# Performance work log

Measured on AMD Instinct MI355X. Metric: run time of the kernel, lower is better.

Reference implementation:

```python
import jax, jax.numpy as jnp
import numpy as np

EPS = 1e-5

def conv(x, w, groups=1):
    # x: NCHW, w: OIHW, VALID padding, stride 1 (cross-correlation, same as torch conv2d)
    return jax.lax.conv_general_dilated(x, w, (1, 1), 'VALID',
                                        feature_group_count=groups,
                                        dimension_numbers=('NCHW', 'OIHW', 'NCHW'))

def bn(x, g, b, m, v):
    # eval-mode batchnorm with running stats
    scale = (g / jnp.sqrt(v + EPS))[None, :, None, None]
    return (x - m[None, :, None, None]) * scale + b[None, :, None, None]

def xcorr_depthwise(x, k):
    # x: [B,C,Hs,Ws] search, k: [B,C,Hk,Wk] per-sample kernels
    B, C, H, W = x.shape
    xr = x.reshape(1, B * C, H, W)
    kr = k.reshape(B * C, 1, k.shape[2], k.shape[3])
    out = conv(xr, kr, groups=B * C)  # [1, B*C, Ho, Wo]
    return out.reshape(B, C, out.shape[2], out.shape[3])

def setup_inputs() -> dict:
    key = jax.random.key(0)
    ks = jax.random.split(key, 16)
    Cin, Hid, Cout = 256, 256, 20
    inp = {
        'kernel': jax.random.normal(ks[0], (128, Cin, 7, 7), jnp.float32),
        'search': jax.random.normal(ks[1], (128, Cin, 31, 31), jnp.float32),
        'wk': jax.random.normal(ks[2], (Hid, Cin, 3, 3), jnp.float32) * 0.02,
        'gk': jnp.ones((Hid,), jnp.float32),
        'bk': jnp.zeros((Hid,), jnp.float32),
        'mk': jax.random.normal(ks[3], (Hid,), jnp.float32) * 0.1,
        'vk': jax.random.uniform(ks[4], (Hid,), jnp.float32) + 0.5,
        'ws': jax.random.normal(ks[5], (Hid, Cin, 3, 3), jnp.float32) * 0.02,
        'gs': jnp.ones((Hid,), jnp.float32),
        'bs': jnp.zeros((Hid,), jnp.float32),
        'ms': jax.random.normal(ks[6], (Hid,), jnp.float32) * 0.1,
        'vs': jax.random.uniform(ks[7], (Hid,), jnp.float32) + 0.5,
        'wh1': jax.random.normal(ks[8], (Hid, Hid, 1, 1), jnp.float32) * 0.02,
        'gh': jnp.ones((Hid,), jnp.float32),
        'bh': jnp.zeros((Hid,), jnp.float32),
        'mh': jax.random.normal(ks[9], (Hid,), jnp.float32) * 0.1,
        'vh': jax.random.uniform(ks[10], (Hid,), jnp.float32) + 0.5,
        'wh2': jax.random.normal(ks[11], (Cout, Hid, 1, 1), jnp.float32) * 0.02,
        'bh2': jnp.zeros((Cout,), jnp.float32),
    }
    return inp

def reference(kernel, search, wk, gk, bk, mk, vk, ws, gs, bs, ms, vs,
              wh1, gh, bh, mh, vh, wh2, bh2):
    k = jax.nn.relu(bn(conv(kernel, wk), gk, bk, mk, vk))   # [B,256,5,5]
    s = jax.nn.relu(bn(conv(search, ws), gs, bs, ms, vs))   # [B,256,29,29]
    f = xcorr_depthwise(s, k)                               # [B,256,25,25]
    h = jax.nn.relu(bn(conv(f, wh1), gh, bh, mh, vh))
    out = conv(h, wh2) + bh2[None, :, None, None]           # [B,20,25,25]
    return out
```

## Files before the change

### kernel.cpp

```cpp
#include <hip/hip_runtime.h>

typedef __bf16 bf16x8 __attribute__((ext_vector_type(8)));
typedef float floatx4 __attribute__((ext_vector_type(4)));
typedef unsigned short u16;
typedef unsigned int u32;

__device__ __forceinline__ u16 f2bf(float f) {
    union { float f; unsigned int u; } q; q.f = f;
    unsigned int r = q.u + 0x7FFFu + ((q.u >> 16) & 1u);
    return (u16)(r >> 16);
}
__device__ __forceinline__ float bf2f(u16 b) {
    union { unsigned int u; float f; } q; q.u = ((unsigned int)b) << 16;
    return q.f;
}

__device__ __forceinline__ void gl2lds16(const u16* g, u16* l) {
    __builtin_amdgcn_global_load_lds((const __attribute__((address_space(1))) u32*)g,
                                     (__attribute__((address_space(3))) u32*)l, 16, 0, 0);
}

__global__ __launch_bounds__(256) void prep_and_transpose(
    const float* __restrict__ kin, u16* __restrict__ KIN,
    const float* __restrict__ sin_, u16* __restrict__ SIN,
    const float* __restrict__ wk, const float* __restrict__ wsw, const float* __restrict__ wh1,
    const float* __restrict__ gk, const float* __restrict__ bk,
    const float* __restrict__ mk, const float* __restrict__ vk,
    const float* __restrict__ gs, const float* __restrict__ bs,
    const float* __restrict__ ms, const float* __restrict__ vs,
    const float* __restrict__ gh, const float* __restrict__ bh,
    const float* __restrict__ mh, const float* __restrict__ vh,
    u16* __restrict__ WKP, u16* __restrict__ WSP, u16* __restrict__ WH1P,
    float* __restrict__ par)
{
    __shared__ float tile[64][33];
    int bid = blockIdx.x, t = threadIdx.x;
    if (bid < 16896) {
        const float* in; u16* out; int HW, sptiles;
        if (bid < 1024) { in = kin;  out = KIN; HW = 49;  sptiles = 2; }
        else { bid -= 1024; in = sin_; out = SIN; HW = 961; sptiles = 31; }
        int st  = bid % sptiles;
        int tmp = bid / sptiles;
        int ct  = tmp & 3;
        int b   = tmp >> 2;
        int sp0 = st * 32, ci0 = ct * 64;
        int j = t & 31, i8 = t >> 5;
        const float* ip = in + ((size_t)b * 256 + ci0 + i8) * HW + sp0 + j;
#pragma unroll
        for (int k = 0; k < 8; ++k) {
            if (sp0 + j < HW) tile[i8 + k * 8][j] = ip[(size_t)(k * 8) * HW];
        }
        __syncthreads();
        int cl = t & 63, s4 = t >> 6;
#pragma unroll
        for (int k = 0; k < 8; ++k) {
            int spl = s4 + k * 4;
            int sp  = sp0 + spl;
            if (sp < HW) out[((size_t)b * HW + sp) * 256 + ci0 + cl] = f2bf(tile[cl][spl]);
        }
        return;
    }
    bid -= 16896;
    if (bid < 4608) {
        const float* src = (bid < 2304) ? wk : wsw;
        u16* dst = (bid < 2304) ? WKP : WSP;
        int tid = ((bid < 2304) ? bid : bid - 2304) * 256 + t;
        int o  = tid / 2304;
        int k  = tid - o * 2304;
        int rc = k >> 8;
        int ci = k & 255;
        dst[tid] = f2bf(src[o * 2304 + ci * 9 + rc]);
    } else if (bid < 4864) {
        int tid = (bid - 4608) * 256 + t;
        WH1P[tid] = f2bf(wh1[tid]);
    } else {
        float s;
        s = gk[t] * rsqrtf(vk[t] + 1e-5f); par[0*256+t] = s; par[1*256+t] = bk[t] - mk[t]*s;
        s = gs[t] * rsqrtf(vs[t] + 1e-5f); par[2*256+t] = s; par[3*256+t] = bs[t] - ms[t]*s;
        s = gh[t] * rsqrtf(vh[t] + 1e-5f); par[4*256+t] = s; par[5*256+t] = bh[t] - mh[t]*s;
    }
}

__global__ __launch_bounds__(256) void conv_gemm(
    const u16* __restrict__ Ain, const u16* __restrict__ Wpk,
    const float* __restrict__ scale, const float* __restrict__ shift,
    u16* __restrict__ Out,
    int OHW, int OW, int IW, int bstride, int KW, int nrc, int mblocks)
{
    __shared__ u16 Alds[4096];
    __shared__ u16 Blds[4096];

    const int tot = mblocks * 2;
    const int grp = (tot >> 3) << 3;
    const int lid = blockIdx.x;
    const int nid = (lid < grp) ? ((lid & 7) * (grp >> 3) + (lid >> 3)) : lid;
    const int m0 = (nid >> 1) * 128;
    const int n0 = (nid & 1) * 128;

    const int t    = threadIdx.x;
    const int wave = t >> 6;
    const int lane = t & 63;
    const int quad = lane >> 4;
    const int lrow = lane & 15;

    const int koff = (((t & 3) ^ ((t >> 3) & 3)) << 3);
    const int r0 = t >> 2;
    int m_a0 = m0 + r0;
    int b0 = m_a0 / OHW; int rem0 = m_a0 - b0 * OHW; int y0 = rem0 / OW; int x0 = rem0 - y0 * OW;
    int m_a1 = m_a0 + 64;
    int b1 = m_a1 / OHW; int rem1 = m_a1 - b1 * OHW; int y1 = rem1 / OW; int x1 = rem1 - y1 * OW;
    const u16* ag0 = Ain + (size_t)b0 * bstride + (size_t)(y0 * IW + x0) * 256 + koff;
    const u16* ag1 = Ain + (size_t)b1 * bstride + (size_t)(y1 * IW + x1) * 256 + koff;
    const int Ktot = nrc * 256;
    const u16* bg0 = Wpk + (size_t)(n0 + r0) * Ktot + koff;
    const u16* bg1 = bg0 + (size_t)64 * Ktot;

    u16* lA0 = Alds + wave * 512;
    u16* lA1 = Alds + 2048 + wave * 512;
    u16* lB0 = Blds + wave * 512;
    u16* lB1 = Blds + 2048 + wave * 512;

    floatx4 zero = {0.f, 0.f, 0.f, 0.f};
    floatx4 acc[4][4];
#pragma unroll
    for (int i = 0; i < 4; ++i)
#pragma unroll
        for (int j = 0; j < 4; ++j) acc[i][j] = zero;

    const int wr  = (wave >> 1) << 6;
    const int wc  = (wave & 1) << 6;
    const int pos = ((quad ^ ((lrow >> 1) & 3)) << 3);

    const int nchunks = nrc << 3;
    for (int ch = 0; ch < nchunks; ++ch) {
        int rc  = ch >> 3;
        int ci0 = (ch & 7) << 5;
        int rr  = rc / KW;
        int cc  = rc - rr * KW;
        int ao  = (rr * IW + cc) * 256 + ci0;
        int bo  = ch << 5;
        __syncthreads();
        gl2lds16(ag0 + ao, lA0);
        gl2lds16(ag1 + ao, lA1);
        gl2lds16(bg0 + bo, lB0);
        gl2lds16(bg1 + bo, lB1);
        __syncthreads();
        bf16x8 af[4], bfr[4];
#pragma unroll
        for (int mi = 0; mi < 4; ++mi)
            af[mi] = *(const bf16x8*)&Alds[(wr + mi * 16 + lrow) * 32 + pos];
#pragma unroll
        for (int ni = 0; ni < 4; ++ni)
            bfr[ni] = *(const bf16x8*)&Blds[(wc + ni * 16 + lrow) * 32 + pos];
#pragma unroll
        for (int mi = 0; mi < 4; ++mi)
#pragma unroll
            for (int ni = 0; ni < 4; ++ni)
                acc[mi][ni] = __builtin_amdgcn_mfma_f32_16x16x32_bf16(af[mi], bfr[ni], acc[mi][ni], 0, 0, 0);
    }

    float sc[4], sh[4];
#pragma unroll
    for (int ni = 0; ni < 4; ++ni) {
        int gn = n0 + wc + ni * 16 + lrow;
        sc[ni] = scale[gn];
        sh[ni] = shift[gn];
    }
#pragma unroll
    for (int mi = 0; mi < 4; ++mi) {
        int gm = m0 + wr + mi * 16 + (quad << 2);
#pragma unroll
        for (int ri = 0; ri < 4; ++ri) {
            size_t ro = (size_t)(gm + ri) * 256 + n0 + wc + lrow;
#pragma unroll
            for (int ni = 0; ni < 4; ++ni) {
                float v = acc[mi][ni][ri] * sc[ni] + sh[ni];
                v = fmaxf(v, 0.f);
                Out[ro + ni * 16] = f2bf(v);
            }
        }
    }
}

#define NS_BLK 421
__global__ __launch_bounds__(512, 2) void conv_gemm256(
    const u16* __restrict__ AinS, const u16* __restrict__ WpkS,
    const float* __restrict__ parS, u16* __restrict__ OutS,
    const u16* __restrict__ AinK, const u16* __restrict__ WpkK,
    const float* __restrict__ parK, u16* __restrict__ OutK)
{
    __shared__ __align__(16) u16 Alds[2][256][64];
    __shared__ __align__(16) u16 Blds[2][256][64];

    const int Ktot = 2304;
    const int NKT  = 36;
    const int KW   = 3;

    const int lid = blockIdx.x;
    const bool isk = (lid >= NS_BLK);

    int nid;
    if (!isk) {
        const int xcd = lid & 7, sub = lid >> 3;
        nid = (xcd < 5) ? (xcd * 53 + sub) : (265 + (xcd - 5) * 52 + sub);
    } else {
        nid = lid - NS_BLK;
    }
    const int m0 = nid << 8;

    const int OHW     = isk ? 25    : 841;
    const int OW      = isk ? 5     : 29;
    const int IW      = isk ? 7     : 31;
    const int bstride = isk ? 12544 : 246016;
    const int Mtot    = isk ? 3200  : 107648;
    const u16* Ain    = isk ? AinK : AinS;
    const u16* Wpk    = isk ? WpkK : WpkS;
    const float* scale = isk ? parK : parS;
    const float* shift = scale + 256;
    u16* Out          = isk ? OutK : OutS;

    const int t     = threadIdx.x;
    const int wave  = t >> 6;
    const int lane  = t & 63;
    const int lrow  = lane & 15;
    const int lquad = lane >> 4;
    const int wmBase = (wave >> 2) << 7;
    const int wnBase = (wave & 3) << 6;

    const u16* pA[4];
    const u16* pB[4];
#pragma unroll
    for (int j = 0; j < 4; ++j) {
        int u = j * 512 + t;
        int row = u >> 3, slot = u & 7;
        int ko = ((slot ^ (row & 7)) << 3);
        int m = m0 + row; if (m >= Mtot) m = Mtot - 1;
        int b = m / OHW; int rem = m - b * OHW; int y = rem / OW; int x = rem - y * OW;
        pA[j] = Ain + (size_t)b * bstride + (size_t)(y * IW + x) * 256 + ko;
        pB[j] = Wpk + (size_t)row * (size_t)Ktot + ko;
    }

    const int xo0 = ((lquad ^ (lrow & 7)) << 3);
    const int xo1 = xo0 ^ 32;

    floatx4 acc[8][4];
#pragma unroll
    for (int i = 0; i < 8; ++i)
#pragma unroll
        for (int j = 0; j < 4; ++j) acc[i][j] = (floatx4){0.f, 0.f, 0.f, 0.f};

#pragma unroll
    for (int j = 0; j < 4; ++j)
        gl2lds16(pA[j], &Alds[0][0][0] + j * 4096 + wave * 512);
#pragma unroll
    for (int j = 0; j < 4; ++j)
        gl2lds16(pB[j], &Blds[0][0][0] + j * 4096 + wave * 512);
    asm volatile("s_waitcnt vmcnt(0)" ::: "memory");
    __builtin_amdgcn_s_barrier();

#define LOADA(mb) do {                                              \
        const u16* _p = Ab + (wmBase + (mb) * 16 + lrow) * 64;      \
        aF[0][0] = *(const bf16x8*)(_p + xo0);                      \
        aF[0][1] = *(const bf16x8*)(_p + xo1);                      \
        aF[1][0] = *(const bf16x8*)(_p + 1024 + xo0);               \
        aF[1][1] = *(const bf16x8*)(_p + 1024 + xo1);               \
    } while (0)

#define MFMA16(mb) do {                                                                               \
        _Pragma("unroll")                                                                             \
        for (int _n = 0; _n < 4; ++_n) {                                                              \
            acc[(mb)][_n]     = __builtin_amdgcn_mfma_f32_16x16x32_bf16(aF[0][0], bB[_n][0], acc[(mb)][_n], 0, 0, 0);     \
            acc[(mb)][_n]     = __builtin_amdgcn_mfma_f32_16x16x32_bf16(aF[0][1], bB[_n][1], acc[(mb)][_n], 0, 0, 0);     \
            acc[(mb) + 1][_n] = __builtin_amdgcn_mfma_f32_16x16x32_bf16(aF[1][0], bB[_n][0], acc[(mb) + 1][_n], 0, 0, 0); \
            acc[(mb) + 1][_n] = __builtin_amdgcn_mfma_f32_16x16x32_bf16(aF[1][1], bB[_n][1], acc[(mb) + 1][_n], 0, 0, 0); \
        }                                                                                             \
    } while (0)

#pragma unroll 2
    for (int kt = 0; kt < NKT; ++kt) {
        const int c = kt & 1;
        const u16* Ab = &Alds[c][0][0];
        const u16* Bb = &Blds[c][0][0];
        u16* An = &Alds[c ^ 1][0][0];
        u16* Bn = &Blds[c ^ 1][0][0];
        const int pf = (kt + 1 < NKT);
        const int kt1 = kt + 1;
        const int rc = kt1 >> 2;
        const int rr = rc / KW;
        const int cc = rc - rr * KW;
        const int aoffA = (rr * IW + cc) * 256 + ((kt1 & 3) << 6);
        const int boffB = kt1 << 6;

        if (pf) {
#pragma unroll
            for (int j = 0; j < 4; ++j)
                gl2lds16(pA[j] + aoffA, An + j * 4096 + wave * 512);
#pragma unroll
            for (int j = 0; j < 4; ++j)
                gl2lds16(pB[j] + boffB, Bn + j * 4096 + wave * 512);
        }

        bf16x8 bB[4][2];
        bf16x8 aF[2][2];
#pragma unroll
        for (int ni = 0; ni < 4; ++ni) {
            const u16* _p = Bb + (wnBase + ni * 16 + lrow) * 64;
            bB[ni][0] = *(const bf16x8*)(_p + xo0);
            bB[ni][1] = *(const bf16x8*)(_p + xo1);
        }
        LOADA(0);
        MFMA16(0);
        LOADA(2);
        MFMA16(2);
        LOADA(4);
        MFMA16(4);
        LOADA(6);
        MFMA16(6);

        asm volatile("s_waitcnt vmcnt(0)" ::: "memory");
        __builtin_amdgcn_s_barrier();
    }

#undef LOADA
#undef MFMA16

    float sc[4], sh[4];
#pragma unroll
    for (int ni = 0; ni < 4; ++ni) {
        int gn = wnBase + ni * 16 + lrow;
        sc[ni] = scale[gn];
        sh[ni] = shift[gn];
    }
#pragma unroll
    for (int mi = 0; mi < 8; ++mi) {
        int gm0 = m0 + wmBase + mi * 16 + (lquad << 2);
#pragma unroll
        for (int ri = 0; ri < 4; ++ri) {
            int gm = gm0 + ri;
            if (gm < Mtot) {
                size_t ro = (size_t)gm * 256 + wnBase + lrow;
#pragma unroll
                for (int ni = 0; ni < 4; ++ni) {
                    float v = acc[mi][ni][ri] * sc[ni] + sh[ni];
                    v = fmaxf(v, 0.f);
                    Out[ro + ni * 16] = f2bf(v);
                }
            }
        }
    }
}

__global__ __launch_bounds__(256) void xcorr(const u16* __restrict__ ss, const u16* __restrict__ kk,
                                             u16* __restrict__ f) {
    int lid = blockIdx.x;
    int bid = (lid & 7) * 400 + (lid >> 3);
    int b = bid / 25, y = bid - b * 25;
    int t = threadIdx.x;
    int cg = (t & 31) << 3;
    int xg = t >> 5;
    const u16* kbase = kk + (size_t)b * 25 * 256 + cg;
    const u16* sbase = ss + (size_t)(b * 29 + y) * 29 * 256 + cg;

    float acc[4][8];
#pragma unroll
    for (int j = 0; j < 4; ++j)
#pragma unroll
        for (int e = 0; e < 8; ++e) acc[j][e] = 0.f;

#pragma unroll
    for (int r = 0; r < 5; ++r) {
        const u16* srow = sbase + (size_t)r * 29 * 256;
#pragma unroll
        for (int c = 0; c < 5; ++c) {
            bf16x8 kv = *(const bf16x8*)(kbase + (r * 5 + c) * 256);
            float kf[8];
#pragma unroll
            for (int e = 0; e < 8; ++e) kf[e] = (float)kv[e];
#pragma unroll
            for (int j = 0; j < 4; ++j) {
                int x = xg + 8 * j;
                if (x < 25) {
                    bf16x8 sv = *(const bf16x8*)(srow + (size_t)(x + c) * 256);
#pragma unroll
                    for (int e = 0; e < 8; ++e) acc[j][e] += (float)sv[e] * kf[e];
                }
            }
        }
    }

    u16* fb = f + (size_t)(b * 25 + y) * 25 * 256 + cg;
#pragma unroll
    for (int j = 0; j < 4; ++j) {
        int x = xg + 8 * j;
        if (x < 25) {
            u16 pk[8];
#pragma unroll
            for (int e = 0; e < 8; ++e) pk[e] = f2bf(acc[j][e]);
            *(bf16x8*)(fb + (size_t)x * 256) = *(const bf16x8*)pk;
        }
    }
}

__global__ __launch_bounds__(256) void head(const u16* __restrict__ h, const float* __restrict__ w2,
                                            const float* __restrict__ b2, float* __restrict__ out) {
    __shared__ __align__(16) u16   hl[25 * 264];
    __shared__ __align__(16) float wl[20 * 260];
    int bid = blockIdx.x;
    int b = bid / 25, y = bid - b * 25;
    int t = threadIdx.x;
    const u16* hrow = h + (size_t)(b * 25 + y) * 25 * 256;
    for (int i = t; i < 800; i += 256) {
        int x = i >> 5, c8 = i & 31;
        *(bf16x8*)&hl[x * 264 + c8 * 8] = *(const bf16x8*)&hrow[i * 8];
    }
    for (int i = t; i < 1280; i += 256) {
        int co = i >> 6, c4 = i & 63;
        *(float4*)&wl[co * 260 + c4 * 4] = *(const float4*)&w2[(size_t)co * 256 + c4 * 4];
    }
    __syncthreads();
    for (int o = t; o < 500; o += 256) {
        int x = o / 20, co = o - x * 20;
        float acc = b2[co];
        const u16* hp = &hl[x * 264];
        const float* wp = &wl[co * 260];
#pragma unroll 4
        for (int k = 0; k < 256; k += 8) {
            bf16x8 hv = *(const bf16x8*)(hp + k);
            float4 w0 = *(const float4*)(wp + k);
            float4 w1v = *(const float4*)(wp + k + 4);
            acc += (float)hv[0] * w0.x + (float)hv[1] * w0.y
                 + (float)hv[2] * w0.z + (float)hv[3] * w0.w
                 + (float)hv[4] * w1v.x + (float)hv[5] * w1v.y
                 + (float)hv[6] * w1v.z + (float)hv[7] * w1v.w;
        }
        out[(size_t)((b * 20 + co) * 25 + y) * 25 + x] = acc;
    }
}

#define OFF_SIN  0ull
#define SZ_SIN   62980096ull
#define OFF_KIN  (OFF_SIN + SZ_SIN)
#define SZ_KIN   3211264ull
#define OFF_WKP  (OFF_KIN + SZ_KIN)
#define SZ_WKP   1179648ull
#define OFF_WSP  (OFF_WKP + SZ_WKP)
#define SZ_WSP   1179648ull
#define OFF_WH1P (OFF_WSP + SZ_WSP)
#define SZ_WH1P  131072ull
#define OFF_PAR  (OFF_WH1P + SZ_WH1P)
#define SZ_PAR   8192ull
#define OFF_KK   (OFF_PAR + SZ_PAR)
#define SZ_KK    1638400ull
#define OFF_SS   (OFF_KK + SZ_KK)
#define SZ_SS    55115776ull
#define OFF_F    OFF_SIN
#define OFF_H    OFF_SS

extern "C" void kernel_launch(void* const* d_in, const int* in_sizes, int n_in,
                              void* d_out, int out_size, void* d_ws, size_t ws_size,
                              hipStream_t stream) {
    const float* kin  = (const float*)d_in[0];
    const float* sin_ = (const float*)d_in[1];
    const float* wk   = (const float*)d_in[2];
    const float* gk   = (const float*)d_in[3];
    const float* bk   = (const float*)d_in[4];
    const float* mk   = (const float*)d_in[5];
    const float* vk   = (const float*)d_in[6];
    const float* wsw  = (const float*)d_in[7];
    const float* gs   = (const float*)d_in[8];
    const float* bs   = (const float*)d_in[9];
    const float* ms   = (const float*)d_in[10];
    const float* vs   = (const float*)d_in[11];
    const float* wh1  = (const float*)d_in[12];
    const float* gh   = (const float*)d_in[13];
    const float* bh   = (const float*)d_in[14];
    const float* mh   = (const float*)d_in[15];
    const float* vh   = (const float*)d_in[16];
    const float* wh2  = (const float*)d_in[17];
    const float* bh2  = (const float*)d_in[18];
    float* out = (float*)d_out;

    char* w = (char*)d_ws;
    u16*   SIN  = (u16*)(w + OFF_SIN);
    u16*   KIN  = (u16*)(w + OFF_KIN);
    u16*   WKP  = (u16*)(w + OFF_WKP);
    u16*   WSP  = (u16*)(w + OFF_WSP);
    u16*   WH1P = (u16*)(w + OFF_WH1P);
    float* PAR  = (float*)(w + OFF_PAR);
    u16*   KK   = (u16*)(w + OFF_KK);
    u16*   SS   = (u16*)(w + OFF_SS);
    u16*   F    = (u16*)(w + OFF_F);
    u16*   H    = (u16*)(w + OFF_H);

    prep_and_transpose<<<21761, 256, 0, stream>>>(kin, KIN, sin_, SIN,
                                                  wk, wsw, wh1,
                                                  gk, bk, mk, vk, gs, bs, ms, vs, gh, bh, mh, vh,
                                                  WKP, WSP, WH1P, PAR);

    conv_gemm256<<<434, 512, 0, stream>>>(SIN, WSP, PAR + 512, SS,
                                          KIN, WKP, PAR + 0, KK);
    xcorr<<<3200, 256, 0, stream>>>(SS, KK, F);
    conv_gemm<<<1250, 256, 0, stream>>>(F, WH1P, PAR + 1024, PAR + 1280, H,
                                        625, 25, 25, 160000, 1, 1, 625);
    head<<<3200, 256, 0, stream>>>(H, wh2, bh2, out);

    (void)in_sizes; (void)n_in; (void)out_size; (void)ws_size;
}
```

Measured before the change: 484.9 us.

## Shrink conv GEMM tile to 256x128 with K32 steps for higher occupancy

```diff
diff --git a/kernel.cpp b/kernel.cpp
--- a/kernel.cpp
+++ b/kernel.cpp
@@ -182,19 +182,18 @@
     }
 }
 
-#define NS_BLK 421
-__global__ __launch_bounds__(512, 2) void conv_gemm256(
+#define NS_BLK 842
+__global__ __launch_bounds__(512, 4) void conv_gemm256(
     const u16* __restrict__ AinS, const u16* __restrict__ WpkS,
     const float* __restrict__ parS, u16* __restrict__ OutS,
     const u16* __restrict__ AinK, const u16* __restrict__ WpkK,
     const float* __restrict__ parK, u16* __restrict__ OutK)
 {
-    __shared__ __align__(16) u16 Alds[2][256][64];
-    __shared__ __align__(16) u16 Blds[2][256][64];
+    __shared__ __align__(16) u16 Alds[2][256][32];
+    __shared__ __align__(16) u16 Blds[2][128][32];
 
     const int Ktot = 2304;
-    const int NKT  = 36;
-    const int KW   = 3;
+    const int NKT  = 72;
 
     const int lid = blockIdx.x;
     const bool isk = (lid >= NS_BLK);
@@ -202,11 +201,12 @@
     int nid;
     if (!isk) {
         const int xcd = lid & 7, sub = lid >> 3;
-        nid = (xcd < 5) ? (xcd * 53 + sub) : (265 + (xcd - 5) * 52 + sub);
+        nid = (xcd < 2) ? (xcd * 106 + sub) : (212 + (xcd - 2) * 105 + sub);
     } else {
         nid = lid - NS_BLK;
     }
-    const int m0 = nid << 8;
+    const int m0 = (nid >> 1) << 8;
+    const int n0 = (nid & 1) << 7;
 
     const int OHW     = isk ? 25    : 841;
     const int OW      = isk ? 5     : 29;
@@ -224,57 +224,39 @@
     const int lane  = t & 63;
     const int lrow  = lane & 15;
     const int lquad = lane >> 4;
-    const int wmBase = (wave >> 2) << 7;
-    const int wnBase = (wave & 3) << 6;
-
-    const u16* pA[4];
-    const u16* pB[4];
-#pragma unroll
-    for (int j = 0; j < 4; ++j) {
+    const int wmBase = (wave >> 1) << 6;
+    const int wnBase = (wave & 1) << 6;
+
+    const u16* pA[2];
+#pragma unroll
+    for (int j = 0; j < 2; ++j) {
         int u = j * 512 + t;
-        int row = u >> 3, slot = u & 7;
-        int ko = ((slot ^ (row & 7)) << 3);
+        int row = u >> 2, slot = u & 3;
+        int ko = ((slot ^ (row & 3) ^ ((row >> 2) & 3)) << 3);
         int m = m0 + row; if (m >= Mtot) m = Mtot - 1;
         int b = m / OHW; int rem = m - b * OHW; int y = rem / OW; int x = rem - y * OW;
         pA[j] = Ain + (size_t)b * bstride + (size_t)(y * IW + x) * 256 + ko;
-        pB[j] = Wpk + (size_t)row * (size_t)Ktot + ko;
-    }
-
-    const int xo0 = ((lquad ^ (lrow & 7)) << 3);
-    const int xo1 = xo0 ^ 32;
-
-    floatx4 acc[8][4];
-#pragma unroll
-    for (int i = 0; i < 8; ++i)
+    }
+    const u16* pB;
+    {
+        int row = t >> 2, slot = t & 3;
+        int ko = ((slot ^ (row & 3) ^ ((row >> 2) & 3)) << 3);
+        pB = Wpk + (size_t)(n0 + row) * Ktot + ko;
+    }
+
+    const int xo = ((lquad ^ (lrow & 3) ^ ((lrow >> 2) & 3)) << 3);
+
+    floatx4 acc[4][4];
+#pragma unroll
+    for (int i = 0; i < 4; ++i)
 #pragma unroll
         for (int j = 0; j < 4; ++j) acc[i][j] = (floatx4){0.f, 0.f, 0.f, 0.f};
 
-#pragma unroll
-    for (int j = 0; j < 4; ++j)
-        gl2lds16(pA[j], &Alds[0][0][0] + j * 4096 + wave * 512);
-#pragma unroll
-    for (int j = 0; j < 4; ++j)
-        gl2lds16(pB[j], &Blds[0][0][0] + j * 4096 + wave * 512);
+    gl2lds16(pA[0], &Alds[0][0][0] + 0 * 4096 + wave * 512);
+    gl2lds16(pA[1], &Alds[0][0][0] + 1 * 4096 + wave * 512);
+    gl2lds16(pB,    &Blds[0][0][0] + wave * 512);
     asm volatile("s_waitcnt vmcnt(0)" ::: "memory");
     __builtin_amdgcn_s_barrier();
-
-#define LOADA(mb) do {                                              \
-        const u16* _p = Ab + (wmBase + (mb) * 16 + lrow) * 64;      \
-        aF[0][0] = *(const bf16x8*)(_p + xo0);                      \
-        aF[0][1] = *(const bf16x8*)(_p + xo1);                      \
-        aF[1][0] = *(const bf16x8*)(_p + 1024 + xo0);               \
-        aF[1][1] = *(const bf16x8*)(_p + 1024 + xo1);               \
-    } while (0)
-
-#define MFMA16(mb) do {                                                                               \
-        _Pragma("unroll")                                                                             \
-        for (int _n = 0; _n < 4; ++_n) {                                                              \
-            acc[(mb)][_n]     = __builtin_amdgcn_mfma_f32_16x16x32_bf16(aF[0][0], bB[_n][0], acc[(mb)][_n], 0, 0, 0);     \
-            acc[(mb)][_n]     = __builtin_amdgcn_mfma_f32_16x16x32_bf16(aF[0][1], bB[_n][1], acc[(mb)][_n], 0, 0, 0);     \
-            acc[(mb) + 1][_n] = __builtin_amdgcn_mfma_f32_16x16x32_bf16(aF[1][0], bB[_n][0], acc[(mb) + 1][_n], 0, 0, 0); \
-            acc[(mb) + 1][_n] = __builtin_amdgcn_mfma_f32_16x16x32_bf16(aF[1][1], bB[_n][1], acc[(mb) + 1][_n], 0, 0, 0); \
-        }                                                                                             \
-    } while (0)
 
 #pragma unroll 2
     for (int kt = 0; kt < NKT; ++kt) {
@@ -285,60 +267,50 @@
         u16* Bn = &Blds[c ^ 1][0][0];
         const int pf = (kt + 1 < NKT);
         const int kt1 = kt + 1;
-        const int rc = kt1 >> 2;
-        const int rr = rc / KW;
-        const int cc = rc - rr * KW;
-        const int aoffA = (rr * IW + cc) * 256 + ((kt1 & 3) << 6);
-        const int boffB = kt1 << 6;
+        const int rc = kt1 >> 3;
+        const int rr = rc / 3;
+        const int cc = rc - rr * 3;
+        const int aoff = (rr * IW + cc) * 256 + ((kt1 & 7) << 5);
+        const int boff = kt1 << 5;
 
         if (pf) {
-#pragma unroll
-            for (int j = 0; j < 4; ++j)
-                gl2lds16(pA[j] + aoffA, An + j * 4096 + wave * 512);
-#pragma unroll
-            for (int j = 0; j < 4; ++j)
-                gl2lds16(pB[j] + boffB, Bn + j * 4096 + wave * 512);
-        }
-
-        bf16x8 bB[4][2];
-        bf16x8 aF[2][2];
-#pragma unroll
-        for (int ni = 0; ni < 4; ++ni) {
-            const u16* _p = Bb + (wnBase + ni * 16 + lrow) * 64;
-            bB[ni][0] = *(const bf16x8*)(_p + xo0);
-            bB[ni][1] = *(const bf16x8*)(_p + xo1);
-        }
-        LOADA(0);
-        MFMA16(0);
-        LOADA(2);
-        MFMA16(2);
-        LOADA(4);
-        MFMA16(4);
-        LOADA(6);
-        MFMA16(6);
+            gl2lds16(pA[0] + aoff, An + 0 * 4096 + wave * 512);
+            gl2lds16(pA[1] + aoff, An + 1 * 4096 + wave * 512);
+            gl2lds16(pB + boff,    Bn + wave * 512);
+        }
+
+        bf16x8 bB[4], aF[4];
+#pragma unroll
+        for (int ni = 0; ni < 4; ++ni)
+            bB[ni] = *(const bf16x8*)(Bb + (wnBase + ni * 16 + lrow) * 32 + xo);
+#pragma unroll
+        for (int mi = 0; mi < 4; ++mi)
+            aF[mi] = *(const bf16x8*)(Ab + (wmBase + mi * 16 + lrow) * 32 + xo);
+#pragma unroll
+        for (int mi = 0; mi < 4; ++mi)
+#pragma unroll
+            for (int ni = 0; ni < 4; ++ni)
+                acc[mi][ni] = __builtin_amdgcn_mfma_f32_16x16x32_bf16(aF[mi], bB[ni], acc[mi][ni], 0, 0, 0);
 
         asm volatile("s_waitcnt vmcnt(0)" ::: "memory");
         __builtin_amdgcn_s_barrier();
     }
 
-#undef LOADA
-#undef MFMA16
-
     float sc[4], sh[4];
 #pragma unroll
     for (int ni = 0; ni < 4; ++ni) {
-        int gn = wnBase + ni * 16 + lrow;
+        int gn = n0 + wnBase + ni * 16 + lrow;
         sc[ni] = scale[gn];
         sh[ni] = shift[gn];
     }
 #pragma unroll
-    for (int mi = 0; mi < 8; ++mi) {
+    for (int mi = 0; mi < 4; ++mi) {
         int gm0 = m0 + wmBase + mi * 16 + (lquad << 2);
 #pragma unroll
         for (int ri = 0; ri < 4; ++ri) {
             int gm = gm0 + ri;
             if (gm < Mtot) {
-                size_t ro = (size_t)gm * 256 + wnBase + lrow;
+                size_t ro = (size_t)gm * 256 + n0 + wnBase + lrow;
 #pragma unroll
                 for (int ni = 0; ni < 4; ++ni) {
                     float v = acc[mi][ni][ri] * sc[ni] + sh[ni];
@@ -497,7 +469,7 @@
                                                   gk, bk, mk, vk, gs, bs, ms, vs, gh, bh, mh, vh,
                                                   WKP, WSP, WH1P, PAR);
 
-    conv_gemm256<<<434, 512, 0, stream>>>(SIN, WSP, PAR + 512, SS,
+    conv_gemm256<<<868, 512, 0, stream>>>(SIN, WSP, PAR + 512, SS,
                                           KIN, WKP, PAR + 0, KK);
     xcorr<<<3200, 256, 0, stream>>>(SS, KK, F);
     conv_gemm<<<1250, 256, 0, stream>>>(F, WH1P, PAR + 1024, PAR + 1280, H,
```

After: 500.1 us. 1.03x slower.
